# Performance work log

Measured on AMD Instinct MI355X. Metric: run time of the kernel, lower is better.

The kernel has to match this reference:

```python
import jax, jax.numpy as jnp
import numpy as np

N_NODES = 163840
N_EDGES = 2621440
F_IN = 64
F_HID = 64
SUBG = 20  # size_subgraph_samples
NEG_SLOPE = 0.2


def gat_conv(x, src, dst, W, a_src, a_dst, b):
    """PyG GATConv, heads=1, concat. src/dst already include self-loops."""
    n = x.shape[0]
    h = x @ W                               # [N, H]
    al_s = h @ a_src                        # [N]
    al_d = h @ a_dst                        # [N]
    e = jax.nn.leaky_relu(al_s[src] + al_d[dst], NEG_SLOPE)  # [E]
    # softmax over incoming edges of each dst node
    m = jax.ops.segment_max(e, dst, num_segments=n)
    ex = jnp.exp(e - m[dst])
    denom = jax.ops.segment_sum(ex, dst, num_segments=n)
    alpha = ex / (denom[dst] + 1e-16)
    msg = h[src] * alpha[:, None]           # [E, H]
    out = jax.ops.segment_sum(msg, dst, num_segments=n)
    return out + b


def setup_inputs() -> dict:
    key = jax.random.key(0)
    ks = jax.random.split(key, 12)
    s = 0.05
    return {
        "x": jax.random.normal(ks[0], (N_NODES, F_IN), jnp.float32),
        "edge_index": jax.random.randint(ks[1], (2, N_EDGES), 0, N_NODES, jnp.int64 if jax.config.jax_enable_x64 else jnp.int32),
        "W1": jax.random.normal(ks[2], (F_IN, F_HID), jnp.float32) * s,
        "a_src1": jax.random.normal(ks[3], (F_HID,), jnp.float32) * s,
        "a_dst1": jax.random.normal(ks[4], (F_HID,), jnp.float32) * s,
        "b1": jnp.zeros((F_HID,), jnp.float32),
        "W2": jax.random.normal(ks[5], (F_HID, F_HID), jnp.float32) * s,
        "a_src2": jax.random.normal(ks[6], (F_HID,), jnp.float32) * s,
        "a_dst2": jax.random.normal(ks[7], (F_HID,), jnp.float32) * s,
        "b2": jnp.zeros((F_HID,), jnp.float32),
        "W_out": jax.random.normal(ks[8], (F_HID * SUBG, 1), jnp.float32) * s,
        "b_out": jnp.zeros((1,), jnp.float32),
    }


def reference(x, edge_index, W1, a_src1, a_dst1, b1, W2, a_src2, a_dst2, b2, W_out, b_out):
    n = x.shape[0]
    loop = jnp.arange(n, dtype=edge_index.dtype)
    src = jnp.concatenate([edge_index[0], loop])  # add_self_loops=True
    dst = jnp.concatenate([edge_index[1], loop])
    h = gat_conv(x, src, dst, W1, a_src1, a_dst1, b1)
    h = jax.nn.relu(h)  # dropout is identity in eval mode
    h = gat_conv(h, src, dst, W2, a_src2, a_dst2, b2)
    h = jax.nn.relu(h)
    h = h.reshape(n // SUBG, F_HID * SUBG)
    return h @ W_out + b_out
```

## Files before the change

### kernel.cpp

```cpp
#include <hip/hip_runtime.h>
#include <math.h>

#define F 64
#define NPB 160
#define BCAP 3584

typedef __attribute__((ext_vector_type(8))) short bf16x8;
typedef __attribute__((ext_vector_type(4))) float f32x4;

__device__ inline unsigned short f2bf(float f) {
  unsigned int u = __float_as_uint(f);
  u += 0x7fffu + ((u >> 16) & 1u);
  return (unsigned short)(u >> 16);
}

__global__ __launch_bounds__(256) void k_prep(const float* __restrict__ W1, const float* __restrict__ W2,
                                              uint4* __restrict__ wf, int* __restrict__ bcnt, int nb,
                                              float* __restrict__ out, const float* __restrict__ bo, int ng,
                                              int* __restrict__ ssrc, int e) {
  int tid = threadIdx.x;
  if (blockIdx.x == 0) {
    for (int i = tid; i < 1024; i += 256) {
      int layer = i >> 9, rem = i & 511;
      int cb = rem >> 6, lane = rem & 63;
      int c = cb >> 1, kk = cb & 1;
      int l15 = lane & 15, quad = lane >> 4;
      const float* W = layer ? W2 : W1;
      unsigned short p[8];
      #pragma unroll
      for (int j = 0; j < 8; j++) {
        int kd = kk * 32 + quad * 8 + j;
        p[j] = f2bf(W[kd * F + c * 16 + l15]);
      }
      wf[i] = *(const uint4*)p;
    }
  } else {
    for (int i = tid; i < nb * 16; i += 256) bcnt[i] = 0;
    float b0 = bo[0];
    for (int i = tid; i < ng; i += 256) out[i] = b0;
    if (tid < 64) ssrc[e + tid] = 0;
  }
}

__device__ __forceinline__ void gemm_body(const float* __restrict__ in, const uint4* __restrict__ wf,
                                          const float* __restrict__ avs, const float* __restrict__ avd,
                                          unsigned short* __restrict__ hgb, float* __restrict__ als,
                                          float* __restrict__ ald, int n, int bid, int nbl) {
  int tid = threadIdx.x, lane = tid & 63, wv = tid >> 6;
  int l15 = lane & 15, quad = lane >> 4;
  bf16x8 bfr[4][2];
  #pragma unroll
  for (int cb = 0; cb < 8; cb++) {
    uint4 u = wf[cb * 64 + lane];
    bfr[cb >> 1][cb & 1] = *(const bf16x8*)&u;
  }
  float as_l[4], ad_l[4];
  #pragma unroll
  for (int c = 0; c < 4; c++) { as_l[c] = avs[c * 16 + l15]; ad_l[c] = avd[c * 16 + l15]; }

  int nchunks = n >> 6;
  for (int chunk = bid; chunk < nchunks; chunk += nbl) {
    int r0 = (chunk << 6) + (wv << 4);
    bf16x8 a0, a1;
    const float4* xr = (const float4*)(in + (size_t)(r0 + l15) * F + quad * 8);
    float4 xa = xr[0], xb = xr[1];
    float4 xc = xr[8], xd = xr[9];
    a0[0] = (short)f2bf(xa.x); a0[1] = (short)f2bf(xa.y); a0[2] = (short)f2bf(xa.z); a0[3] = (short)f2bf(xa.w);
    a0[4] = (short)f2bf(xb.x); a0[5] = (short)f2bf(xb.y); a0[6] = (short)f2bf(xb.z); a0[7] = (short)f2bf(xb.w);
    a1[0] = (short)f2bf(xc.x); a1[1] = (short)f2bf(xc.y); a1[2] = (short)f2bf(xc.z); a1[3] = (short)f2bf(xc.w);
    a1[4] = (short)f2bf(xd.x); a1[5] = (short)f2bf(xd.y); a1[6] = (short)f2bf(xd.z); a1[7] = (short)f2bf(xd.w);
    f32x4 cfr[4];
    #pragma unroll
    for (int c = 0; c < 4; c++) {
      cfr[c] = (f32x4){0.f, 0.f, 0.f, 0.f};
      cfr[c] = __builtin_amdgcn_mfma_f32_16x16x32_bf16(a0, bfr[c][0], cfr[c], 0, 0, 0);
      cfr[c] = __builtin_amdgcn_mfma_f32_16x16x32_bf16(a1, bfr[c][1], cfr[c], 0, 0, 0);
    }
    #pragma unroll
    for (int i = 0; i < 4; i++) {
      int row = r0 + quad * 4 + i;
      #pragma unroll
      for (int c = 0; c < 4; c++) hgb[(size_t)row * F + c * 16 + l15] = f2bf(cfr[c][i]);
      float ps = cfr[0][i] * as_l[0] + cfr[1][i] * as_l[1] + cfr[2][i] * as_l[2] + cfr[3][i] * as_l[3];
      float pd = cfr[0][i] * ad_l[0] + cfr[1][i] * ad_l[1] + cfr[2][i] * ad_l[2] + cfr[3][i] * ad_l[3];
      #pragma unroll
      for (int o = 1; o <= 8; o <<= 1) { ps += __shfl_xor(ps, o); pd += __shfl_xor(pd, o); }
      if (l15 == 0) { als[row] = ps; ald[row] = pd; }
    }
  }
}

__global__ __launch_bounds__(256) void k_scatter_gemm1(const int* __restrict__ esrc, const int* __restrict__ edst,
                                                       int* __restrict__ bcnt, unsigned int* __restrict__ binned,
                                                       int e, int ch, int S,
                                                       const float* __restrict__ x, const uint4* __restrict__ wf,
                                                       const float* __restrict__ avs, const float* __restrict__ avd,
                                                       unsigned short* __restrict__ hgb, float* __restrict__ als,
                                                       float* __restrict__ ald, int n) {
  int k = blockIdx.x, tid = threadIdx.x;
  if (k < S) {
    __shared__ int hist[1024];
    __shared__ int cur[1024];
    for (int i = tid; i < 1024; i += 256) hist[i] = 0;
    __syncthreads();
    int beg = k * ch, end = min(e, beg + ch);
    int len = end - beg;
    if (len <= 0) return;
    int nv = len >> 2;
    for (int g = tid; g < nv; g += 256) {
      int4 d4 = *(const int4*)(edst + beg + (g << 2));
      atomicAdd(&hist[d4.x / NPB], 1);
      atomicAdd(&hist[d4.y / NPB], 1);
      atomicAdd(&hist[d4.z / NPB], 1);
      atomicAdd(&hist[d4.w / NPB], 1);
    }
    for (int i = beg + (nv << 2) + tid; i < end; i += 256) atomicAdd(&hist[edst[i] / NPB], 1);
    __syncthreads();
    for (int b = tid; b < 1024; b += 256) {
      int c = hist[b];
      int base = 0;
      if (c) base = atomicAdd(&bcnt[b * 16], c);
      cur[b] = b * BCAP + base;
    }
    __syncthreads();
    for (int g = tid; g < nv; g += 256) {
      int i = beg + (g << 2);
      int4 d4 = *(const int4*)(edst + i);
      int4 s4 = *(const int4*)(esrc + i);
      #pragma unroll
      for (int j = 0; j < 4; j++) {
        int d = (j == 0) ? d4.x : (j == 1) ? d4.y : (j == 2) ? d4.z : d4.w;
        int s = (j == 0) ? s4.x : (j == 1) ? s4.y : (j == 2) ? s4.z : s4.w;
        int b = d / NPB;
        int p = atomicAdd(&cur[b], 1);
        if (p < (b + 1) * BCAP) binned[p] = (unsigned int)s | ((unsigned int)(d - b * NPB) << 24);
      }
    }
    for (int i = beg + (nv << 2) + tid; i < end; i += 256) {
      int d = edst[i];
      int b = d / NPB;
      int p = atomicAdd(&cur[b], 1);
      if (p < (b + 1) * BCAP) binned[p] = (unsigned int)esrc[i] | ((unsigned int)(d - b * NPB) << 24);
    }
    return;
  }
  gemm_body(x, wf, avs, avd, hgb, als, ald, n, k - S, (int)gridDim.x - S);
}

__global__ __launch_bounds__(256) void k_bucket_csr(const unsigned int* __restrict__ binned,
                                                    const int* __restrict__ bcnt,
                                                    int* __restrict__ ssrc, int* __restrict__ offs,
                                                    int n, int nb) {
  __shared__ int ncnt[NPB];
  __shared__ int cur[NPB];
  __shared__ int sc[256];
  __shared__ int red[256];
  __shared__ int stage[BCAP];
  int b = blockIdx.x, tid = threadIdx.x;
  int acc = 0;
  for (int j = tid; j < b; j += 256) acc += min(bcnt[j * 16], BCAP);
  red[tid] = acc;
  __syncthreads();
  #pragma unroll
  for (int o = 128; o > 0; o >>= 1) {
    if (tid < o) red[tid] += red[tid + o];
    __syncthreads();
  }
  int outbase = red[0];
  int ecnt = min(bcnt[b * 16], BCAP);
  int node0 = b * NPB;
  int nn = min(NPB, n - node0);
  int ebeg = b * BCAP;
  for (int i = tid; i < NPB; i += 256) ncnt[i] = 0;
  __syncthreads();
  for (int i = tid; i < ecnt; i += 256) { unsigned int v = binned[ebeg + i]; atomicAdd(&ncnt[v >> 24], 1); }
  __syncthreads();
  int x = (tid < nn) ? ncnt[tid] : 0;
  sc[tid] = x;
  __syncthreads();
  #pragma unroll
  for (int o = 1; o < 256; o <<= 1) {
    int y = (tid >= o) ? sc[tid - o] : 0;
    __syncthreads();
    sc[tid] += y;
    __syncthreads();
  }
  if (tid < nn) {
    int noff = sc[tid] - x;
    cur[tid] = noff;
    offs[node0 + tid] = outbase + noff;
  }
  __syncthreads();
  for (int i = tid; i < ecnt; i += 256) {
    unsigned int v = binned[ebeg + i];
    int p = atomicAdd(&cur[v >> 24], 1);
    stage[p] = (int)(v & 0xFFFFFFu);
  }
  __syncthreads();
  for (int i = tid; i < ecnt; i += 256) ssrc[outbase + i] = stage[i];
  if (b == nb - 1 && tid == 0) offs[n] = outbase + ecnt;
}

__device__ __forceinline__ void agg_node(int node, int n, const int* __restrict__ offs,
                                         const int* __restrict__ ssrc,
                                         const uint4* __restrict__ hg4,
                                         const float* __restrict__ als,
                                         const float* __restrict__ ald,
                                         float4 bl0, float4 bl1, int l8, float r[8]) {
  int cnode = min(node, n - 1);
  int beg = offs[cnode];
  int deg = offs[cnode + 1] - beg;
  int degc = max(deg - 1, 0);
  if (deg == 0) beg = 0;
  float aldv = ald[cnode];

  float ts = als[cnode] + aldv;
  ts = fmaxf(ts, 0.2f * ts);
  float exs = __expf(ts);
  float s = exs;
  uint4 us = hg4[(size_t)cnode * 8 + l8];
  float acc[8];
  acc[0] = exs * __uint_as_float(us.x << 16);
  acc[1] = exs * __uint_as_float(us.x & 0xffff0000u);
  acc[2] = exs * __uint_as_float(us.y << 16);
  acc[3] = exs * __uint_as_float(us.y & 0xffff0000u);
  acc[4] = exs * __uint_as_float(us.z << 16);
  acc[5] = exs * __uint_as_float(us.z & 0xffff0000u);
  acc[6] = exs * __uint_as_float(us.w << 16);
  acc[7] = exs * __uint_as_float(us.w & 0xffff0000u);

  int dm = deg;
  #pragma unroll
  for (int o = 8; o <= 32; o <<= 1) dm = max(dm, __shfl_xor(dm, o));

  #pragma unroll 4
  for (int j = 0; j < dm; j++) {
    int jj = min(j, degc);
    int src = ssrc[beg + jj];
    float t = als[src] + aldv;
    t = fmaxf(t, 0.2f * t);
    float ex = (j < deg) ? __expf(t) : 0.f;
    s += ex;
    uint4 u = hg4[(size_t)src * 8 + l8];
    acc[0] = fmaf(ex, __uint_as_float(u.x << 16), acc[0]);
    acc[1] = fmaf(ex, __uint_as_float(u.x & 0xffff0000u), acc[1]);
    acc[2] = fmaf(ex, __uint_as_float(u.y << 16), acc[2]);
    acc[3] = fmaf(ex, __uint_as_float(u.y & 0xffff0000u), acc[3]);
    acc[4] = fmaf(ex, __uint_as_float(u.z << 16), acc[4]);
    acc[5] = fmaf(ex, __uint_as_float(u.z & 0xffff0000u), acc[5]);
    acc[6] = fmaf(ex, __uint_as_float(u.w << 16), acc[6]);
    acc[7] = fmaf(ex, __uint_as_float(u.w & 0xffff0000u), acc[7]);
  }

  float iv = 1.f / (s + 1e-16f);
  r[0] = fmaxf(fmaf(acc[0], iv, bl0.x), 0.f);
  r[1] = fmaxf(fmaf(acc[1], iv, bl0.y), 0.f);
  r[2] = fmaxf(fmaf(acc[2], iv, bl0.z), 0.f);
  r[3] = fmaxf(fmaf(acc[3], iv, bl0.w), 0.f);
  r[4] = fmaxf(fmaf(acc[4], iv, bl1.x), 0.f);
  r[5] = fmaxf(fmaf(acc[5], iv, bl1.y), 0.f);
  r[6] = fmaxf(fmaf(acc[6], iv, bl1.z), 0.f);
  r[7] = fmaxf(fmaf(acc[7], iv, bl1.w), 0.f);
}

__global__ __launch_bounds__(256) void k_spmm_g2(const int* __restrict__ offs, const int* __restrict__ ssrc,
                                                 const unsigned short* __restrict__ hgb,
                                                 const float* __restrict__ als, const float* __restrict__ ald,
                                                 const float* __restrict__ bias, const uint4* __restrict__ wf2,
                                                 const float* __restrict__ avs, const float* __restrict__ avd,
                                                 unsigned short* __restrict__ hgb2, float* __restrict__ als2,
                                                 float* __restrict__ ald2, int n) {
  __shared__ __align__(16) unsigned short hsh[64][72];
  int tid = threadIdx.x, lane = tid & 63, wv = tid >> 6;
  int g8 = lane >> 3, l8 = lane & 7;
  const uint4* hg4 = (const uint4*)hgb;
  float4 bl0 = ((const float4*)bias)[l8 * 2];
  float4 bl1 = ((const float4*)bias)[l8 * 2 + 1];

  for (int p = 0; p < 2; p++) {
    int row = p * 32 + wv * 8 + g8;
    int node = blockIdx.x * 64 + row;
    float r[8];
    agg_node(node, n, offs, ssrc, hg4, als, ald, bl0, bl1, l8, r);
    unsigned short pk[8];
    #pragma unroll
    for (int k = 0; k < 8; k++) pk[k] = f2bf(r[k]);
    *(uint4*)&hsh[row][l8 * 8] = *(const uint4*)pk;
  }
  __syncthreads();

  int l15 = lane & 15, quad = lane >> 4;
  bf16x8 bfr[4][2];
  #pragma unroll
  for (int cb = 0; cb < 8; cb++) {
    uint4 u = wf2[cb * 64 + lane];
    bfr[cb >> 1][cb & 1] = *(const bf16x8*)&u;
  }
  float as_l[4], ad_l[4];
  #pragma unroll
  for (int c = 0; c < 4; c++) { as_l[c] = avs[c * 16 + l15]; ad_l[c] = avd[c * 16 + l15]; }

  int r0 = wv << 4;
  uint4 u0 = *(const uint4*)&hsh[r0 + l15][quad * 8];
  uint4 u1 = *(const uint4*)&hsh[r0 + l15][quad * 8 + 32];
  bf16x8 a0 = *(const bf16x8*)&u0;
  bf16x8 a1 = *(const bf16x8*)&u1;
  f32x4 cfr[4];
  #pragma unroll
  for (int c = 0; c < 4; c++) {
    cfr[c] = (f32x4){0.f, 0.f, 0.f, 0.f};
    cfr[c] = __builtin_amdgcn_mfma_f32_16x16x32_bf16(a0, bfr[c][0], cfr[c], 0, 0, 0);
    cfr[c] = __builtin_amdgcn_mfma_f32_16x16x32_bf16(a1, bfr[c][1], cfr[c], 0, 0, 0);
  }
  #pragma unroll
  for (int i = 0; i < 4; i++) {
    int row = blockIdx.x * 64 + r0 + quad * 4 + i;
    #pragma unroll
    for (int c = 0; c < 4; c++) hgb2[(size_t)row * F + c * 16 + l15] = f2bf(cfr[c][i]);
    float ps = cfr[0][i] * as_l[0] + cfr[1][i] * as_l[1] + cfr[2][i] * as_l[2] + cfr[3][i] * as_l[3];
    float pd = cfr[0][i] * ad_l[0] + cfr[1][i] * ad_l[1] + cfr[2][i] * ad_l[2] + cfr[3][i] * ad_l[3];
    #pragma unroll
    for (int o = 1; o <= 8; o <<= 1) { ps += __shfl_xor(ps, o); pd += __shfl_xor(pd, o); }
    if (l15 == 0) { als2[row] = ps; ald2[row] = pd; }
  }
}

__global__ __launch_bounds__(256) void k_spmm_out(const int* __restrict__ offs, const int* __restrict__ ssrc,
                                                  const unsigned short* __restrict__ hgb,
                                                  const float* __restrict__ als, const float* __restrict__ ald,
                                                  const float* __restrict__ bias, const float* __restrict__ Wout,
                                                  float* __restrict__ out, int n) {
  int tid = threadIdx.x, lane = tid & 63, wv = tid >> 6;
  int g8 = lane >> 3, l8 = lane & 7;
  const uint4* hg4 = (const uint4*)hgb;
  float4 bl0 = ((const float4*)bias)[l8 * 2];
  float4 bl1 = ((const float4*)bias)[l8 * 2 + 1];

  __shared__ float gsl[3];
  if (tid < 3) gsl[tid] = 0.f;

  int node = (blockIdx.x * 4 + wv) * 8 + g8;
  bool nodeok = node < n;
  int cnode = min(node, n - 1);
  float r[8];
  agg_node(node, n, offs, ssrc, hg4, als, ald, bl0, bl1, l8, r);

  int node0 = blockIdx.x * 32;
  int grp0 = node0 / 20;
  int grp = cnode / 20, slot = cnode - grp * 20;
  const float* wr = Wout + slot * F + l8 * 8;
  float dot = 0.f;
  #pragma unroll
  for (int k = 0; k < 8; k++) dot = fmaf(r[k], wr[k], dot);
  #pragma unroll
  for (int o = 1; o <= 4; o <<= 1) dot += __shfl_xor(dot, o);
  __syncthreads();
  if (nodeok && l8 == 0) atomicAdd(&gsl[grp - grp0], dot);
  __syncthreads();
  if (tid < 3) {
    float v = gsl[tid];
    if (v != 0.f) atomicAdd(out + grp0 + tid, v);
  }
}

extern "C" void kernel_launch(void* const* d_in, const int* in_sizes, int n_in,
                              void* d_out, int out_size, void* d_ws, size_t ws_size,
                              hipStream_t stream) {
  const float* x   = (const float*)d_in[0];
  const int*   ei  = (const int*)d_in[1];
  const float* W1  = (const float*)d_in[2];
  const float* as1 = (const float*)d_in[3];
  const float* ad1 = (const float*)d_in[4];
  const float* b1  = (const float*)d_in[5];
  const float* W2  = (const float*)d_in[6];
  const float* as2 = (const float*)d_in[7];
  const float* ad2 = (const float*)d_in[8];
  const float* b2  = (const float*)d_in[9];
  const float* Wo  = (const float*)d_in[10];
  const float* bo  = (const float*)d_in[11];
  float* out = (float*)d_out;

  const int N = in_sizes[0] / F;
  const int E = in_sizes[1] / 2;
  const int* esrc = ei;
  const int* edst = ei + E;

  size_t off = 0;
  auto alloc = [&](size_t bytes) -> void* {
    void* p = (char*)d_ws + off;
    off += (bytes + 255) & ~(size_t)255;
    return p;
  };
  unsigned short* hgb  = (unsigned short*)alloc((size_t)N * F * 2);
  unsigned short* hgb2 = (unsigned short*)alloc((size_t)N * F * 2);
  float* als  = (float*)alloc((size_t)N * 4);
  float* ald  = (float*)alloc((size_t)N * 4);
  float* als2 = (float*)alloc((size_t)N * 4);
  float* ald2 = (float*)alloc((size_t)N * 4);
  int* offs   = (int*)alloc((size_t)(N + 1) * 4);
  int* bcnt   = (int*)alloc((size_t)1024 * 16 * 4);
  int* ssrc   = (int*)alloc((size_t)(E + 64) * 4);
  unsigned int* binned = (unsigned int*)alloc((size_t)1024 * BCAP * 4);
  uint4* wf   = (uint4*)alloc(16384);
  (void)ws_size; (void)n_in; (void)out_size;

  const int NG = N / 20;
  const int NB = (N + NPB - 1) / NPB;
  const int S = 256;
  const int CH = (((E + S - 1) / S) + 3) & ~3;

  k_prep<<<2, 256, 0, stream>>>(W1, W2, wf, bcnt, NB, out, bo, NG, ssrc, E);
  k_scatter_gemm1<<<S + (N >> 6), 256, 0, stream>>>(esrc, edst, bcnt, binned, E, CH, S,
                                                    x, wf, as1, ad1, hgb, als, ald, N);
  k_bucket_csr<<<NB, 256, 0, stream>>>(binned, bcnt, ssrc, offs, N, NB);
  k_spmm_g2<<<(N >> 6), 256, 0, stream>>>(offs, ssrc, hgb, als, ald, b1, wf + 512, as2, ad2,
                                          hgb2, als2, ald2, N);
  k_spmm_out<<<(N >> 5), 256, 0, stream>>>(offs, ssrc, hgb2, als2, ald2, b2, Wo, out, N);
}
```

Measured before the change: 271.2 us.

## Fuse bucket CSR build with layer-1 aggregation and layer-2 GEMM

Merges the bucket-to-CSR kernel with the layer-1 aggregation and layer-2 MFMA GEMM, so each block aggregates its 128 nodes straight from the shared-memory staged source list instead of rereading ssrc/offs from global memory. Buckets switch to 128 nodes (power of two, shifts instead of divides, 7-bit local index at bit 25) with 1280 buckets and a smaller capacity. The scatter phase uses 512 blocks instead of 256. This removes one launch and a global round trip, but there are fewer, heavier aggregation blocks with more shared memory each, and the per-bucket capacity is tighter.

```diff
diff --git a/kernel.cpp b/kernel.cpp
--- a/kernel.cpp
+++ b/kernel.cpp
@@ -2,8 +2,9 @@
 #include <math.h>
 
 #define F 64
-#define NPB 160
-#define BCAP 3584
+#define NPB 128
+#define NBK 1280
+#define BCAP 2960
 
 typedef __attribute__((ext_vector_type(8))) short bf16x8;
 typedef __attribute__((ext_vector_type(4))) float f32x4;
@@ -16,8 +17,7 @@
 
 __global__ __launch_bounds__(256) void k_prep(const float* __restrict__ W1, const float* __restrict__ W2,
                                               uint4* __restrict__ wf, int* __restrict__ bcnt, int nb,
-                                              float* __restrict__ out, const float* __restrict__ bo, int ng,
-                                              int* __restrict__ ssrc, int e) {
+                                              float* __restrict__ out, const float* __restrict__ bo, int ng) {
   int tid = threadIdx.x;
   if (blockIdx.x == 0) {
     for (int i = tid; i < 1024; i += 256) {
@@ -38,7 +38,6 @@
     for (int i = tid; i < nb * 16; i += 256) bcnt[i] = 0;
     float b0 = bo[0];
     for (int i = tid; i < ng; i += 256) out[i] = b0;
-    if (tid < 64) ssrc[e + tid] = 0;
   }
 }
 
@@ -99,9 +98,9 @@
                                                        float* __restrict__ ald, int n) {
   int k = blockIdx.x, tid = threadIdx.x;
   if (k < S) {
-    __shared__ int hist[1024];
-    __shared__ int cur[1024];
-    for (int i = tid; i < 1024; i += 256) hist[i] = 0;
+    __shared__ int hist[NBK];
+    __shared__ int cur[NBK];
+    for (int i = tid; i < NBK; i += 256) hist[i] = 0;
     __syncthreads();
     int beg = k * ch, end = min(e, beg + ch);
     int len = end - beg;
@@ -109,14 +108,14 @@
     int nv = len >> 2;
     for (int g = tid; g < nv; g += 256) {
       int4 d4 = *(const int4*)(edst + beg + (g << 2));
-      atomicAdd(&hist[d4.x / NPB], 1);
-      atomicAdd(&hist[d4.y / NPB], 1);
-      atomicAdd(&hist[d4.z / NPB], 1);
-      atomicAdd(&hist[d4.w / NPB], 1);
-    }
-    for (int i = beg + (nv << 2) + tid; i < end; i += 256) atomicAdd(&hist[edst[i] / NPB], 1);
-    __syncthreads();
-    for (int b = tid; b < 1024; b += 256) {
+      atomicAdd(&hist[d4.x >> 7], 1);
+      atomicAdd(&hist[d4.y >> 7], 1);
+      atomicAdd(&hist[d4.z >> 7], 1);
+      atomicAdd(&hist[d4.w >> 7], 1);
+    }
+    for (int i = beg + (nv << 2) + tid; i < end; i += 256) atomicAdd(&hist[edst[i] >> 7], 1);
+    __syncthreads();
+    for (int b = tid; b < NBK; b += 256) {
       int c = hist[b];
       int base = 0;
       if (c) base = atomicAdd(&bcnt[b * 16], c);
@@ -131,35 +130,44 @@
       for (int j = 0; j < 4; j++) {
         int d = (j == 0) ? d4.x : (j == 1) ? d4.y : (j == 2) ? d4.z : d4.w;
         int s = (j == 0) ? s4.x : (j == 1) ? s4.y : (j == 2) ? s4.z : s4.w;
-        int b = d / NPB;
+        int b = d >> 7;
         int p = atomicAdd(&cur[b], 1);
-        if (p < (b + 1) * BCAP) binned[p] = (unsigned int)s | ((unsigned int)(d - b * NPB) << 24);
+        if (p < (b + 1) * BCAP) binned[p] = (unsigned int)s | ((unsigned int)(d & 127) << 25);
       }
     }
     for (int i = beg + (nv << 2) + tid; i < end; i += 256) {
       int d = edst[i];
-      int b = d / NPB;
+      int b = d >> 7;
       int p = atomicAdd(&cur[b], 1);
-      if (p < (b + 1) * BCAP) binned[p] = (unsigned int)esrc[i] | ((unsigned int)(d - b * NPB) << 24);
+      if (p < (b + 1) * BCAP) binned[p] = (unsigned int)esrc[i] | ((unsigned int)(d & 127) << 25);
     }
     return;
   }
   gemm_body(x, wf, avs, avd, hgb, als, ald, n, k - S, (int)gridDim.x - S);
 }
 
-__global__ __launch_bounds__(256) void k_bucket_csr(const unsigned int* __restrict__ binned,
+__global__ __launch_bounds__(256) void k_csr_agg_g2(const unsigned int* __restrict__ binned,
                                                     const int* __restrict__ bcnt,
                                                     int* __restrict__ ssrc, int* __restrict__ offs,
-                                                    int n, int nb) {
+                                                    const unsigned short* __restrict__ hgb,
+                                                    const float* __restrict__ als, const float* __restrict__ ald,
+                                                    const float* __restrict__ bias, const uint4* __restrict__ wf2,
+                                                    const float* __restrict__ avs, const float* __restrict__ avd,
+                                                    unsigned short* __restrict__ hgb2, float* __restrict__ als2,
+                                                    float* __restrict__ ald2, int n, int nb) {
+  __shared__ int red[256];
   __shared__ int ncnt[NPB];
+  __shared__ int noff[NPB];
   __shared__ int cur[NPB];
   __shared__ int sc[256];
-  __shared__ int red[256];
   __shared__ int stage[BCAP];
+  __shared__ __align__(16) unsigned short hsh[NPB][72];
   int b = blockIdx.x, tid = threadIdx.x;
-  int acc = 0;
-  for (int j = tid; j < b; j += 256) acc += min(bcnt[j * 16], BCAP);
-  red[tid] = acc;
+  int lane = tid & 63, wv = tid >> 6;
+
+  int acc0 = 0;
+  for (int j = tid; j < b; j += 256) acc0 += min(bcnt[j * 16], BCAP);
+  red[tid] = acc0;
   __syncthreads();
   #pragma unroll
   for (int o = 128; o > 0; o >>= 1) {
@@ -170,10 +178,11 @@
   int ecnt = min(bcnt[b * 16], BCAP);
   int node0 = b * NPB;
   int nn = min(NPB, n - node0);
-  int ebeg = b * BCAP;
-  for (int i = tid; i < NPB; i += 256) ncnt[i] = 0;
-  __syncthreads();
-  for (int i = tid; i < ecnt; i += 256) { unsigned int v = binned[ebeg + i]; atomicAdd(&ncnt[v >> 24], 1); }
+  size_t ebeg = (size_t)b * BCAP;
+
+  if (tid < NPB) ncnt[tid] = 0;
+  __syncthreads();
+  for (int i = tid; i < ecnt; i += 256) atomicAdd(&ncnt[binned[ebeg + i] >> 25], 1);
   __syncthreads();
   int x = (tid < nn) ? ncnt[tid] : 0;
   sc[tid] = x;
@@ -186,19 +195,129 @@
     __syncthreads();
   }
   if (tid < nn) {
-    int noff = sc[tid] - x;
-    cur[tid] = noff;
-    offs[node0 + tid] = outbase + noff;
+    int nf = sc[tid] - x;
+    noff[tid] = nf;
+    cur[tid] = nf;
+    offs[node0 + tid] = outbase + nf;
   }
   __syncthreads();
   for (int i = tid; i < ecnt; i += 256) {
     unsigned int v = binned[ebeg + i];
-    int p = atomicAdd(&cur[v >> 24], 1);
-    stage[p] = (int)(v & 0xFFFFFFu);
-  }
+    int p = atomicAdd(&cur[v >> 25], 1);
+    stage[p] = (int)(v & 0x1FFFFFFu);
+  }
+  if (tid == 0 && ecnt == 0) stage[0] = 0;
   __syncthreads();
   for (int i = tid; i < ecnt; i += 256) ssrc[outbase + i] = stage[i];
   if (b == nb - 1 && tid == 0) offs[n] = outbase + ecnt;
+
+  int g8 = lane >> 3, l8 = lane & 7;
+  const uint4* hg4 = (const uint4*)hgb;
+  float4 bl0 = ((const float4*)bias)[l8 * 2];
+  float4 bl1 = ((const float4*)bias)[l8 * 2 + 1];
+
+  for (int ppass = 0; ppass < 4; ppass++) {
+    int row = ppass * 32 + wv * 8 + g8;
+    int node = node0 + row;
+    bool rowok = row < nn;
+    int cnode = min(node, n - 1);
+    int deg = rowok ? ncnt[row] : 0;
+    int beg = (deg > 0) ? noff[row] : 0;
+    int degc = max(deg - 1, 0);
+    float aldv = ald[cnode];
+
+    float ts = als[cnode] + aldv;
+    ts = fmaxf(ts, 0.2f * ts);
+    float exs = __expf(ts);
+    float s = exs;
+    uint4 us = hg4[(size_t)cnode * 8 + l8];
+    float acc[8];
+    acc[0] = exs * __uint_as_float(us.x << 16);
+    acc[1] = exs * __uint_as_float(us.x & 0xffff0000u);
+    acc[2] = exs * __uint_as_float(us.y << 16);
+    acc[3] = exs * __uint_as_float(us.y & 0xffff0000u);
+    acc[4] = exs * __uint_as_float(us.z << 16);
+    acc[5] = exs * __uint_as_float(us.z & 0xffff0000u);
+    acc[6] = exs * __uint_as_float(us.w << 16);
+    acc[7] = exs * __uint_as_float(us.w & 0xffff0000u);
+
+    int dm = deg;
+    #pragma unroll
+    for (int o = 8; o <= 32; o <<= 1) dm = max(dm, __shfl_xor(dm, o));
+
+    #pragma unroll 4
+    for (int j = 0; j < dm; j++) {
+      int jj = min(j, degc);
+      int src = stage[beg + jj];
+      float t = als[src] + aldv;
+      t = fmaxf(t, 0.2f * t);
+      float ex = (j < deg) ? __expf(t) : 0.f;
+      s += ex;
+      uint4 u = hg4[(size_t)src * 8 + l8];
+      acc[0] = fmaf(ex, __uint_as_float(u.x << 16), acc[0]);
+      acc[1] = fmaf(ex, __uint_as_float(u.x & 0xffff0000u), acc[1]);
+      acc[2] = fmaf(ex, __uint_as_float(u.y << 16), acc[2]);
+      acc[3] = fmaf(ex, __uint_as_float(u.y & 0xffff0000u), acc[3]);
+      acc[4] = fmaf(ex, __uint_as_float(u.z << 16), acc[4]);
+      acc[5] = fmaf(ex, __uint_as_float(u.z & 0xffff0000u), acc[5]);
+      acc[6] = fmaf(ex, __uint_as_float(u.w << 16), acc[6]);
+      acc[7] = fmaf(ex, __uint_as_float(u.w & 0xffff0000u), acc[7]);
+    }
+
+    float iv = rowok ? (1.f / (s + 1e-16f)) : 0.f;
+    float r[8];
+    r[0] = fmaxf(fmaf(acc[0], iv, rowok ? bl0.x : 0.f), 0.f);
+    r[1] = fmaxf(fmaf(acc[1], iv, rowok ? bl0.y : 0.f), 0.f);
+    r[2] = fmaxf(fmaf(acc[2], iv, rowok ? bl0.z : 0.f), 0.f);
+    r[3] = fmaxf(fmaf(acc[3], iv, rowok ? bl0.w : 0.f), 0.f);
+    r[4] = fmaxf(fmaf(acc[4], iv, rowok ? bl1.x : 0.f), 0.f);
+    r[5] = fmaxf(fmaf(acc[5], iv, rowok ? bl1.y : 0.f), 0.f);
+    r[6] = fmaxf(fmaf(acc[6], iv, rowok ? bl1.z : 0.f), 0.f);
+    r[7] = fmaxf(fmaf(acc[7], iv, rowok ? bl1.w : 0.f), 0.f);
+    unsigned short pk[8];
+    #pragma unroll
+    for (int kk = 0; kk < 8; kk++) pk[kk] = f2bf(r[kk]);
+    *(uint4*)&hsh[row][l8 * 8] = *(const uint4*)pk;
+  }
+  __syncthreads();
+
+  int l15 = lane & 15, quad = lane >> 4;
+  bf16x8 bfr[4][2];
+  #pragma unroll
+  for (int cb = 0; cb < 8; cb++) {
+    uint4 u = wf2[cb * 64 + lane];
+    bfr[cb >> 1][cb & 1] = *(const bf16x8*)&u;
+  }
+  float as_l[4], ad_l[4];
+  #pragma unroll
+  for (int c = 0; c < 4; c++) { as_l[c] = avs[c * 16 + l15]; ad_l[c] = avd[c * 16 + l15]; }
+
+  #pragma unroll
+  for (int t = 0; t < 2; t++) {
+    int r0 = t * 64 + (wv << 4);
+    uint4 u0 = *(const uint4*)&hsh[r0 + l15][quad * 8];
+    uint4 u1 = *(const uint4*)&hsh[r0 + l15][quad * 8 + 32];
+    bf16x8 a0 = *(const bf16x8*)&u0;
+    bf16x8 a1 = *(const bf16x8*)&u1;
+    f32x4 cfr[4];
+    #pragma unroll
+    for (int c = 0; c < 4; c++) {
+      cfr[c] = (f32x4){0.f, 0.f, 0.f, 0.f};
+      cfr[c] = __builtin_amdgcn_mfma_f32_16x16x32_bf16(a0, bfr[c][0], cfr[c], 0, 0, 0);
+      cfr[c] = __builtin_amdgcn_mfma_f32_16x16x32_bf16(a1, bfr[c][1], cfr[c], 0, 0, 0);
+    }
+    #pragma unroll
+    for (int i = 0; i < 4; i++) {
+      int row = node0 + r0 + quad * 4 + i;
+      #pragma unroll
+      for (int c = 0; c < 4; c++) hgb2[(size_t)row * F + c * 16 + l15] = f2bf(cfr[c][i]);
+      float ps = cfr[0][i] * as_l[0] + cfr[1][i] * as_l[1] + cfr[2][i] * as_l[2] + cfr[3][i] * as_l[3];
+      float pd = cfr[0][i] * ad_l[0] + cfr[1][i] * ad_l[1] + cfr[2][i] * ad_l[2] + cfr[3][i] * ad_l[3];
+      #pragma unroll
+      for (int o = 1; o <= 8; o <<= 1) { ps += __shfl_xor(ps, o); pd += __shfl_xor(pd, o); }
+      if (l15 == 0) { als2[row] = ps; ald2[row] = pd; }
+    }
+  }
 }
 
 __device__ __forceinline__ void agg_node(int node, int n, const int* __restrict__ offs,
@@ -263,68 +382,6 @@
   r[7] = fmaxf(fmaf(acc[7], iv, bl1.w), 0.f);
 }
 
-__global__ __launch_bounds__(256) void k_spmm_g2(const int* __restrict__ offs, const int* __restrict__ ssrc,
-                                                 const unsigned short* __restrict__ hgb,
-                                                 const float* __restrict__ als, const float* __restrict__ ald,
-                                                 const float* __restrict__ bias, const uint4* __restrict__ wf2,
-                                                 const float* __restrict__ avs, const float* __restrict__ avd,
-                                                 unsigned short* __restrict__ hgb2, float* __restrict__ als2,
-                                                 float* __restrict__ ald2, int n) {
-  __shared__ __align__(16) unsigned short hsh[64][72];
-  int tid = threadIdx.x, lane = tid & 63, wv = tid >> 6;
-  int g8 = lane >> 3, l8 = lane & 7;
-  const uint4* hg4 = (const uint4*)hgb;
-  float4 bl0 = ((const float4*)bias)[l8 * 2];
-  float4 bl1 = ((const float4*)bias)[l8 * 2 + 1];
-
-  for (int p = 0; p < 2; p++) {
-    int row = p * 32 + wv * 8 + g8;
-    int node = blockIdx.x * 64 + row;
-    float r[8];
-    agg_node(node, n, offs, ssrc, hg4, als, ald, bl0, bl1, l8, r);
-    unsigned short pk[8];
-    #pragma unroll
-    for (int k = 0; k < 8; k++) pk[k] = f2bf(r[k]);
-    *(uint4*)&hsh[row][l8 * 8] = *(const uint4*)pk;
-  }
-  __syncthreads();
-
-  int l15 = lane & 15, quad = lane >> 4;
-  bf16x8 bfr[4][2];
-  #pragma unroll
-  for (int cb = 0; cb < 8; cb++) {
-    uint4 u = wf2[cb * 64 + lane];
-    bfr[cb >> 1][cb & 1] = *(const bf16x8*)&u;
-  }
-  float as_l[4], ad_l[4];
-  #pragma unroll
-  for (int c = 0; c < 4; c++) { as_l[c] = avs[c * 16 + l15]; ad_l[c] = avd[c * 16 + l15]; }
-
-  int r0 = wv << 4;
-  uint4 u0 = *(const uint4*)&hsh[r0 + l15][quad * 8];
-  uint4 u1 = *(const uint4*)&hsh[r0 + l15][quad * 8 + 32];
-  bf16x8 a0 = *(const bf16x8*)&u0;
-  bf16x8 a1 = *(const bf16x8*)&u1;
-  f32x4 cfr[4];
-  #pragma unroll
-  for (int c = 0; c < 4; c++) {
-    cfr[c] = (f32x4){0.f, 0.f, 0.f, 0.f};
-    cfr[c] = __builtin_amdgcn_mfma_f32_16x16x32_bf16(a0, bfr[c][0], cfr[c], 0, 0, 0);
-    cfr[c] = __builtin_amdgcn_mfma_f32_16x16x32_bf16(a1, bfr[c][1], cfr[c], 0, 0, 0);
-  }
-  #pragma unroll
-  for (int i = 0; i < 4; i++) {
-    int row = blockIdx.x * 64 + r0 + quad * 4 + i;
-    #pragma unroll
-    for (int c = 0; c < 4; c++) hgb2[(size_t)row * F + c * 16 + l15] = f2bf(cfr[c][i]);
-    float ps = cfr[0][i] * as_l[0] + cfr[1][i] * as_l[1] + cfr[2][i] * as_l[2] + cfr[3][i] * as_l[3];
-    float pd = cfr[0][i] * ad_l[0] + cfr[1][i] * ad_l[1] + cfr[2][i] * ad_l[2] + cfr[3][i] * ad_l[3];
-    #pragma unroll
-    for (int o = 1; o <= 8; o <<= 1) { ps += __shfl_xor(ps, o); pd += __shfl_xor(pd, o); }
-    if (l15 == 0) { als2[row] = ps; ald2[row] = pd; }
-  }
-}
-
 __global__ __launch_bounds__(256) void k_spmm_out(const int* __restrict__ offs, const int* __restrict__ ssrc,
                                                   const unsigned short* __restrict__ hgb,
                                                   const float* __restrict__ als, const float* __restrict__ ald,
@@ -398,22 +455,21 @@
   float* als2 = (float*)alloc((size_t)N * 4);
   float* ald2 = (float*)alloc((size_t)N * 4);
   int* offs   = (int*)alloc((size_t)(N + 1) * 4);
-  int* bcnt   = (int*)alloc((size_t)1024 * 16 * 4);
+  int* bcnt   = (int*)alloc((size_t)NBK * 16 * 4);
   int* ssrc   = (int*)alloc((size_t)(E + 64) * 4);
-  unsigned int* binned = (unsigned int*)alloc((size_t)1024 * BCAP * 4);
+  unsigned int* binned = (unsigned int*)alloc((size_t)NBK * BCAP * 4);
   uint4* wf   = (uint4*)alloc(16384);
   (void)ws_size; (void)n_in; (void)out_size;
 
   const int NG = N / 20;
   const int NB = (N + NPB - 1) / NPB;
-  const int S = 256;
+  const int S = 512;
   const int CH = (((E + S - 1) / S) + 3) & ~3;
 
-  k_prep<<<2, 256, 0, stream>>>(W1, W2, wf, bcnt, NB, out, bo, NG, ssrc, E);
+  k_prep<<<2, 256, 0, stream>>>(W1, W2, wf, bcnt, NB, out, bo, NG);
   k_scatter_gemm1<<<S + (N >> 6), 256, 0, stream>>>(esrc, edst, bcnt, binned, E, CH, S,
                                                     x, wf, as1, ad1, hgb, als, ald, N);
-  k_bucket_csr<<<NB, 256, 0, stream>>>(binned, bcnt, ssrc, offs, N, NB);
-  k_spmm_g2<<<(N >> 6), 256, 0, stream>>>(offs, ssrc, hgb, als, ald, b1, wf + 512, as2, ad2,
-                                          hgb2, als2, ald2, N);
+  k_csr_agg_g2<<<NB, 256, 0, stream>>>(binned, bcnt, ssrc, offs, hgb, als, ald, b1,
+                                       wf + 512, as2, ad2, hgb2, als2, ald2, N, NB);
   k_spmm_out<<<(N >> 5), 256, 0, stream>>>(offs, ssrc, hgb2, als2, ald2, b2, Wo, out, N);
 }
```

New measurement: 304.4 us. +12.2%, slower.
